# Kernel optimization log

Hardware: AMD Instinct MI355X
Metric: run time of the kernel (lower is better)

Reference implementation:

```python
import jax, jax.numpy as jnp
import numpy as np

N_HEAD = 16
D_MODEL = 1024
D_K = D_MODEL // N_HEAD  # 64
NEG = -1000000000.0


def setup_inputs() -> dict:
    key = jax.random.key(0)
    ks = jax.random.split(key, 7)
    B, L = 4, 2048
    q = jax.random.normal(ks[0], (B, L, D_MODEL), dtype=jnp.float32)
    k = jax.random.normal(ks[1], (B, L, D_MODEL), dtype=jnp.float32)
    v = jax.random.normal(ks[2], (B, L, D_MODEL), dtype=jnp.float32)
    mask = jnp.ones((B, L, L), dtype=jnp.int32)
    s = 1.0 / np.sqrt(D_MODEL)
    w_q = jax.random.normal(ks[3], (D_MODEL, D_MODEL), dtype=jnp.float32) * s
    w_k = jax.random.normal(ks[4], (D_MODEL, D_MODEL), dtype=jnp.float32) * s
    w_v = jax.random.normal(ks[5], (D_MODEL, D_MODEL), dtype=jnp.float32) * s
    w_o = jax.random.normal(ks[6], (D_MODEL, D_MODEL), dtype=jnp.float32) * s
    return {"q": q, "k": k, "v": v, "w_q": w_q, "w_k": w_k, "w_v": w_v, "w_o": w_o, "mask": mask}


def reference(q, k, v, w_q, w_k, w_v, w_o, mask):
    B, Lq, _ = q.shape
    temperature = jnp.asarray(D_K, q.dtype) ** 0.5
    # Projections (Linear, no bias): x @ W^T, then split heads -> [B, H, L, d_k]
    qh = (q @ w_q.T).reshape(B, Lq, N_HEAD, D_K).transpose(0, 2, 1, 3)
    kh = (k @ w_k.T).reshape(B, -1, N_HEAD, D_K).transpose(0, 2, 1, 3)
    vh = (v @ w_v.T).reshape(B, -1, N_HEAD, D_K).transpose(0, 2, 1, 3)
    # Scaled dot-product attention, full [B, H, Lq, Lk] scores materialized
    attn = jnp.einsum("bhqd,bhkd->bhqk", qh / temperature, kh)
    attn = jnp.where(mask[:, None, :, :] == 0, NEG, attn)
    attn = jax.nn.softmax(attn, axis=-1)  # dropout is identity in eval mode
    out = jnp.einsum("bhqk,bhkd->bhqd", attn, vh)
    out = out.transpose(0, 2, 1, 3).reshape(B, Lq, D_MODEL)
    return out @ w_o.T
```

## Files before the change

### kernel.cpp

```cpp
#include <hip/hip_runtime.h>
#include <stdint.h>

typedef float  f32x4  __attribute__((ext_vector_type(4)));
typedef __bf16 bf16x8 __attribute__((ext_vector_type(8)));
typedef __bf16 bf16x4 __attribute__((ext_vector_type(4)));
typedef short  s16x8  __attribute__((ext_vector_type(8)));
typedef short  s16x4  __attribute__((ext_vector_type(4)));
typedef unsigned int   u32;
typedef unsigned short u16;
typedef u32 u32x2 __attribute__((ext_vector_type(2)));

#define DM 1024
#define LQ 2048
#define NH 16

__device__ __forceinline__ u16 f2bf(float f) {
    unsigned int u = __builtin_bit_cast(unsigned int, f);
    u += 0x7FFFu + ((u >> 16) & 1u);
    return (u16)(u >> 16);
}

__device__ __forceinline__ float fexp2(float x) {
#if __has_builtin(__builtin_amdgcn_exp2f)
    return __builtin_amdgcn_exp2f(x);
#else
    return exp2f(x);
#endif
}

__device__ __forceinline__ u32 cvtpk(float lo, float hi) {
    u32 r;
    asm("v_cvt_pk_bf16_f32 %0, %1, %2" : "=v"(r) : "v"(lo), "v"(hi));
    return r;
}

__device__ __forceinline__ float max3f(float a, float b, float c) {
    float r;
    asm("v_max3_f32 %0, %1, %2, %3" : "=v"(r) : "v"(a), "v"(b), "v"(c));
    return r;
}

__device__ __forceinline__ f32x4 mfma32(s16x8 a, s16x8 b, f32x4 c) {
    return __builtin_amdgcn_mfma_f32_16x16x32_bf16(
        __builtin_bit_cast(bf16x8, a), __builtin_bit_cast(bf16x8, b), c, 0, 0, 0);
}

#if __has_builtin(__builtin_amdgcn_mfma_f32_16x16x16_bf16)
__device__ __forceinline__ f32x4 mfma16(s16x4 a, s16x4 b, f32x4 c) {
    return __builtin_amdgcn_mfma_f32_16x16x16_bf16(
        __builtin_bit_cast(bf16x4, a), __builtin_bit_cast(bf16x4, b), c, 0, 0, 0);
}
#else
__device__ __forceinline__ f32x4 mfma16(s16x4 a, s16x4 b, f32x4 c) {
    return __builtin_amdgcn_mfma_f32_16x16x16bf16_1k(a, b, c, 0, 0, 0);
}
#endif

#define GLD16(gp, lp) __builtin_amdgcn_global_load_lds( \
    (__attribute__((address_space(1))) void*)(gp),      \
    (__attribute__((address_space(3))) void*)(lp), 16, 0, 0)

__global__ void k_mask_check(const int4* __restrict__ m4, int n4, int* flag) {
    bool z = false;
    for (int i = blockIdx.x * blockDim.x + threadIdx.x; i < n4;
         i += gridDim.x * blockDim.x) {
        int4 v = m4[i];
        if (v.x == 0 || v.y == 0 || v.z == 0 || v.w == 0) z = true;
    }
    if (__ballot(z)) {
        if ((threadIdx.x & 63) == 0) atomicAnd(flag, 0);
    }
}

__global__ void k_cvt_all(const float4* __restrict__ q,  const float4* __restrict__ k,
                          const float4* __restrict__ v,  const float4* __restrict__ wq,
                          const float4* __restrict__ wk, const float4* __restrict__ wv,
                          const float4* __restrict__ wo,
                          uint64_t* xq, uint64_t* xk, uint64_t* xv,
                          uint64_t* bwq, uint64_t* bwk, uint64_t* bwv, uint64_t* bwo,
                          int* flag)
{
    if (blockIdx.x == 0 && threadIdx.x == 0) *flag = 1;
    const int NX = 2097152, NW = 262144;
    const int total = 3 * NX + 4 * NW;
    const int stride = gridDim.x * blockDim.x;
    for (int idx = blockIdx.x * blockDim.x + threadIdx.x; idx < total; idx += stride) {
        const float4* s; uint64_t* d; int off;
        if (idx < 3 * NX) {
            int ji = idx >> 21;
            off = idx & (NX - 1);
            s = ji == 0 ? q : ji == 1 ? k : v;
            d = ji == 0 ? xq : ji == 1 ? xk : xv;
        } else {
            int r = idx - 3 * NX;
            int ji = r >> 18;
            off = r & (NW - 1);
            s = ji == 0 ? wq : ji == 1 ? wk : ji == 2 ? wv : wo;
            d = ji == 0 ? bwq : ji == 1 ? bwk : ji == 2 ? bwv : bwo;
        }
        float4 f = s[off];
        union { u16 u[4]; uint64_t qq; } rr;
        rr.u[0] = f2bf(f.x); rr.u[1] = f2bf(f.y);
        rr.u[2] = f2bf(f.z); rr.u[3] = f2bf(f.w);
        d[off] = rr.qq;
    }
}

template <int MODE>
__global__ __launch_bounds__(256) void k_gemm(
    const u16* __restrict__ A, const u16* __restrict__ Bw,
    u16* __restrict__ Cb, float* __restrict__ Cf, float scale)
{
    constexpr int K = 1024;
    __shared__ char lA[128 * 32 * 2];
    __shared__ char lB[128 * 32 * 2];
    const int t = threadIdx.x, l = t & 63, w = t >> 6;
    const int q = l & 15, g = l >> 4;
    const int m0 = blockIdx.y * 128, n0 = blockIdx.x * 128;
    const int wr = (w >> 1) * 64, wc = (w & 1) * 64;

    f32x4 acc[4][4];
#pragma unroll
    for (int i = 0; i < 4; i++)
#pragma unroll
        for (int j = 0; j < 4; j++) acc[i][j] = (f32x4){0.f, 0.f, 0.f, 0.f};

    for (int k0 = 0; k0 < K; k0 += 32) {
#pragma unroll
        for (int c = 0; c < 2; c++) {
            int i = c * 256 + t;
            int row = i >> 2, sl = i & 3;
            int ss = sl ^ (row & 3);
            GLD16(A  + (size_t)(m0 + row) * K + k0 + ss * 8, lA + (i - l) * 16);
            GLD16(Bw + (size_t)(n0 + row) * K + k0 + ss * 8, lB + (i - l) * 16);
        }
        __syncthreads();
        s16x8 af[4], bfr[4];
#pragma unroll
        for (int mt = 0; mt < 4; mt++) {
            int r = wr + mt * 16 + q;
            af[mt] = *(const s16x8*)(lA + r * 64 + ((g ^ (r & 3)) * 16));
        }
#pragma unroll
        for (int nt = 0; nt < 4; nt++) {
            int r = wc + nt * 16 + q;
            bfr[nt] = *(const s16x8*)(lB + r * 64 + ((g ^ (r & 3)) * 16));
        }
#pragma unroll
        for (int mt = 0; mt < 4; mt++)
#pragma unroll
            for (int nt = 0; nt < 4; nt++)
                acc[mt][nt] = mfma32(bfr[nt], af[mt], acc[mt][nt]);
        __syncthreads();
    }

#pragma unroll
    for (int mt = 0; mt < 4; mt++) {
        int m = m0 + wr + mt * 16 + q;
#pragma unroll
        for (int nt = 0; nt < 4; nt++) {
            int n = n0 + wc + nt * 16 + g * 4;
            f32x4 a = acc[mt][nt];
            if (MODE == 0) {
                int bb = m >> 11, row = m & 2047;
                int h = n >> 6, d = n & 63;
                s16x4 pk;
#pragma unroll
                for (int j = 0; j < 4; j++) pk[j] = (short)f2bf(a[j] * scale);
                *(s16x4*)(Cb + (((size_t)(bb * NH + h) * LQ + row) << 6) + d) = pk;
            } else {
                f32x4 o;
#pragma unroll
                for (int j = 0; j < 4; j++) o[j] = a[j] * scale;
                *(f32x4*)(Cf + (size_t)m * DM + n) = o;
            }
        }
    }
}

__global__ __launch_bounds__(256, 2) void k_attn(
    const u16* __restrict__ Qh, const u16* __restrict__ Kh,
    const u16* __restrict__ Vh, u16* __restrict__ ctx,
    const int* __restrict__ mask, const int* __restrict__ flag)
{
    __shared__ char lds[32768];
    char* lK0 = lds;
    char* lV0 = lds + 16384;
    const int t = threadIdx.x, l = t & 63, w = t >> 6;
    const int g = l >> 4, q = l & 15;
    const int p = blockIdx.x;
    const int bh = (p & 7) * 8 + ((p >> 3) >> 3);
    const int qt = ((p >> 3) & 7) * 256;
    const int allones = *flag;
    const size_t base = (size_t)bh * LQ * 64;
    const int dg = t & 15, kg = t >> 4;

    s16x8 qf[4][2];
#pragma unroll
    for (int qh = 0; qh < 4; qh++)
#pragma unroll
        for (int kh = 0; kh < 2; kh++)
            qf[qh][kh] = *(const s16x8*)(
                Qh + base + (size_t)(qt + w * 64 + qh * 16 + q) * 64 + kh * 32 + g * 8);

    f32x4 oacc[4][4];
#pragma unroll
    for (int qh = 0; qh < 4; qh++)
#pragma unroll
        for (int dt = 0; dt < 4; dt++) oacc[qh][dt] = (f32x4){0.f, 0.f, 0.f, 0.f};
    float mrow[4] = {-1e30f, -1e30f, -1e30f, -1e30f};
    float lrow[4] = {0.f, 0.f, 0.f, 0.f};

    auto stageK = [&](int kt, int b) {
#pragma unroll
        for (int c = 0; c < 2; c++) {
            int i = c * 256 + t;
            int row = i >> 3, sl = i & 7;
            GLD16(Kh + base + (size_t)(kt + row) * 64 + ((sl ^ (row & 7)) * 8),
                  lK0 + b * 8192 + (i - l) * 16);
        }
    };
    auto loadV = [&](int kt, s16x4* vr) {
#pragma unroll
        for (int j = 0; j < 4; j++)
            vr[j] = *(const s16x4*)(Vh + base + (size_t)(kt + kg * 4 + j) * 64 + dg * 4);
    };
    auto writeV = [&](const s16x4* vr, int b) {
        u32x2 vv[4];
#pragma unroll
        for (int j = 0; j < 4; j++) vv[j] = __builtin_bit_cast(u32x2, vr[j]);
#pragma unroll
        for (int jj = 0; jj < 4; jj++) {
            int d = dg * 4 + jj;
            u32 a0 = vv[0][jj >> 1], a1 = vv[1][jj >> 1];
            u32 a2 = vv[2][jj >> 1], a3 = vv[3][jj >> 1];
            u32 w0, w1;
            if (jj & 1) { w0 = (a0 >> 16) | (a1 & 0xffff0000u);
                          w1 = (a2 >> 16) | (a3 & 0xffff0000u); }
            else        { w0 = (a0 & 0xffffu) | (a1 << 16);
                          w1 = (a2 & 0xffffu) | (a3 << 16); }
            u32x2 pw = {w0, w1};
            *(s16x4*)(lV0 + b * 8192 + d * 128 + ((kg ^ (d & 15)) * 8)) =
                __builtin_bit_cast(s16x4, pw);
        }
    };

    {
        s16x4 vr[4];
        stageK(0, 0);
        loadV(0, vr);
        writeV(vr, 0);
    }

    int cur = 0;
    for (int kt = 0; kt < LQ; kt += 64) {
        __syncthreads();
        const bool more = (kt + 64) < LQ;
        s16x4 vr[4];
        if (more) {
            stageK(kt + 64, cur ^ 1);
            loadV(kt + 64, vr);
        }

        f32x4 sc[4][4];
#pragma unroll
        for (int qh = 0; qh < 4; qh++)
#pragma unroll
            for (int ct = 0; ct < 4; ct++) sc[qh][ct] = (f32x4){0.f, 0.f, 0.f, 0.f};
        __builtin_amdgcn_s_setprio(1);
#pragma unroll
        for (int ct = 0; ct < 4; ct++) {
            int kc = ct * 16 + q;
#pragma unroll
            for (int kh = 0; kh < 2; kh++) {
                s16x8 kf = *(const s16x8*)(lK0 + cur * 8192 + kc * 128 +
                                           (((kh * 4 + g) ^ (kc & 7)) * 16));
#pragma unroll
                for (int qh = 0; qh < 4; qh++)
                    sc[qh][ct] = mfma32(kf, qf[qh][kh], sc[qh][ct]);
            }
        }
        __builtin_amdgcn_s_setprio(0);

        if (!allones) {
            int b = bh >> 4;
#pragma unroll
            for (int qh = 0; qh < 4; qh++)
#pragma unroll
                for (int ct = 0; ct < 4; ct++)
#pragma unroll
                    for (int r = 0; r < 4; r++) {
                        int qr = qt + w * 64 + qh * 16 + q;
                        int kc = kt + ct * 16 + g * 4 + r;
                        if (mask[(size_t)(b * LQ + qr) * LQ + kc] == 0)
                            sc[qh][ct][r] = -1e9f;
                    }
        }

        float pm[4];
#pragma unroll
        for (int qh = 0; qh < 4; qh++) {
            float m0 = max3f(sc[qh][0][0], sc[qh][0][1], sc[qh][0][2]);
            m0 = max3f(m0, sc[qh][0][3], sc[qh][1][0]);
            m0 = max3f(m0, sc[qh][1][1], sc[qh][1][2]);
            m0 = max3f(m0, sc[qh][1][3], sc[qh][2][0]);
            m0 = max3f(m0, sc[qh][2][1], sc[qh][2][2]);
            m0 = max3f(m0, sc[qh][2][3], sc[qh][3][0]);
            m0 = max3f(m0, sc[qh][3][1], sc[qh][3][2]);
            m0 = fmaxf(m0, sc[qh][3][3]);
            m0 = fmaxf(m0, __shfl_xor(m0, 16, 64));
            m0 = fmaxf(m0, __shfl_xor(m0, 32, 64));
            pm[qh] = m0;
        }
        bool ok = pm[0] <= mrow[0] + 8.f;
        ok = ok && (pm[1] <= mrow[1] + 8.f);
        ok = ok && (pm[2] <= mrow[2] + 8.f);
        ok = ok && (pm[3] <= mrow[3] + 8.f);
        if (!__all(ok)) {
#pragma unroll
            for (int qh = 0; qh < 4; qh++) {
                float nm = fmaxf(mrow[qh], pm[qh]);
                float corr = fexp2(mrow[qh] - nm);
                mrow[qh] = nm;
                lrow[qh] *= corr;
                float cv[4];
#pragma unroll
                for (int r = 0; r < 4; r++) cv[r] = __shfl(corr, g * 4 + r, 64);
#pragma unroll
                for (int dt = 0; dt < 4; dt++)
#pragma unroll
                    for (int r = 0; r < 4; r++) oacc[qh][dt][r] *= cv[r];
            }
        }
        s16x4 pa[4][4];
#pragma unroll
        for (int qh = 0; qh < 4; qh++) {
            float rs = 0.f;
#pragma unroll
            for (int ct = 0; ct < 4; ct++)
#pragma unroll
                for (int r = 0; r < 4; r++) {
                    float e = fexp2(sc[qh][ct][r] - mrow[qh]);
                    sc[qh][ct][r] = e;
                    rs += e;
                }
            rs += __shfl_xor(rs, 16, 64);
            rs += __shfl_xor(rs, 32, 64);
            lrow[qh] += rs;
#pragma unroll
            for (int s = 0; s < 4; s++) {
                u32x2 pw;
                pw.x = cvtpk(sc[qh][s][0], sc[qh][s][1]);
                pw.y = cvtpk(sc[qh][s][2], sc[qh][s][3]);
                pa[qh][s] = __builtin_bit_cast(s16x4, pw);
            }
        }

        __builtin_amdgcn_s_setprio(1);
#pragma unroll
        for (int dt = 0; dt < 4; dt++) {
#pragma unroll
            for (int s = 0; s < 4; s++) {
                s16x4 vf = *(const s16x4*)(lV0 + cur * 8192 + (dt * 16 + q) * 128 +
                                           (((s * 4 + g) ^ q) * 8));
#pragma unroll
                for (int qh = 0; qh < 4; qh++)
                    oacc[qh][dt] = mfma16(pa[qh][s], vf, oacc[qh][dt]);
            }
        }
        __builtin_amdgcn_s_setprio(0);

        if (more) writeV(vr, cur ^ 1);
        cur ^= 1;
    }

    __syncthreads();
    char* eb = lds + w * 8192;
#pragma unroll
    for (int qh = 0; qh < 4; qh++) {
        float lv[4];
#pragma unroll
        for (int r = 0; r < 4; r++) lv[r] = 1.f / __shfl(lrow[qh], g * 4 + r, 64);
#pragma unroll
        for (int dt = 0; dt < 4; dt++)
#pragma unroll
            for (int r = 0; r < 4; r++) {
                int row = qh * 16 + g * 4 + r;
                int cb = ((dt * 16 + q) * 2) ^ ((row & 7) << 4);
                *(u16*)(eb + row * 128 + cb) = f2bf(oacc[qh][dt][r] * lv[r]);
            }
    }
    __syncthreads();
    const int b = bh >> 4, h = bh & 15;
    const int token = qt + w * 64 + l;
    u16* gp = ctx + (size_t)(b * LQ + token) * DM + h * 64;
#pragma unroll
    for (int j = 0; j < 8; j++) {
        int cb = (j * 16) ^ ((l & 7) << 4);
        *(s16x8*)(gp + j * 8) = *(const s16x8*)(eb + l * 128 + cb);
    }
}

extern "C" void kernel_launch(void* const* d_in, const int* in_sizes, int n_in,
                              void* d_out, int out_size, void* d_ws, size_t ws_size,
                              hipStream_t stream)
{
    const float* q  = (const float*)d_in[0];
    const float* k  = (const float*)d_in[1];
    const float* v  = (const float*)d_in[2];
    const float* wq = (const float*)d_in[3];
    const float* wk = (const float*)d_in[4];
    const float* wv = (const float*)d_in[5];
    const float* wo = (const float*)d_in[6];
    const int* mask = (const int*)d_in[7];

    char* ws = (char*)d_ws;
    const size_t SX = (size_t)8192 * 1024 * 2;
    const size_t SW = (size_t)1024 * 1024 * 2;
    u16* xq  = (u16*)(ws);
    u16* xk  = (u16*)(ws + SX);
    u16* xv  = (u16*)(ws + 2 * SX);
    u16* bwq = (u16*)(ws + 3 * SX);
    u16* bwk = (u16*)(ws + 3 * SX + SW);
    u16* bwv = (u16*)(ws + 3 * SX + 2 * SW);
    u16* bwo = (u16*)(ws + 3 * SX + 3 * SW);
    u16* Qh  = (u16*)(ws + 3 * SX + 4 * SW);
    u16* Kh  = (u16*)(ws + 4 * SX + 4 * SW);
    u16* Vh  = (u16*)(ws + 5 * SX + 4 * SW);
    u16* ctx = (u16*)(ws + 6 * SX + 4 * SW);
    int* flag = (int*)(ws + 7 * SX + 4 * SW);

    k_cvt_all<<<2048, 256, 0, stream>>>(
        (const float4*)q, (const float4*)k, (const float4*)v,
        (const float4*)wq, (const float4*)wk, (const float4*)wv, (const float4*)wo,
        (uint64_t*)xq, (uint64_t*)xk, (uint64_t*)xv,
        (uint64_t*)bwq, (uint64_t*)bwk, (uint64_t*)bwv, (uint64_t*)bwo, flag);
    k_mask_check<<<2048, 256, 0, stream>>>((const int4*)mask,
                                           (4 * 2048 * 2048) / 4, flag);

    dim3 gg(8, 64);
    k_gemm<0><<<gg, 256, 0, stream>>>(xq, bwq, Qh, nullptr, 0.18033688011112042f);
    k_gemm<0><<<gg, 256, 0, stream>>>(xk, bwk, Kh, nullptr, 1.0f);
    k_gemm<0><<<gg, 256, 0, stream>>>(xv, bwv, Vh, nullptr, 1.0f);

    k_attn<<<512, 256, 0, stream>>>(Qh, Kh, Vh, ctx, mask, flag);

    k_gemm<1><<<gg, 256, 0, stream>>>(ctx, bwo, nullptr, (float*)d_out, 1.0f);
}
```

Measured before the change: 271.1 us.

## Batch QKV projections into one launch, swizzle tile order, use v_perm for V transpose

The three Q/K/V projection GEMMs become a single launch that uses blockIdx.z to pick the input, weight and output, relying on the contiguous workspace layout. The 2D grid is flattened and remapped so consecutive blocks share weight column tiles and nearby rows, which should improve L2 reuse. In the attention kernel's V staging, the shift/mask bf16 interleave becomes v_perm_b32 byte permutes. The intent is to cut launch overhead and tail effects and to trim ALU work, at the cost of depending on fixed buffer strides.

Result: faster. 250.2 us (-7.7%).

```diff
diff --git a/kernel.cpp b/kernel.cpp
--- a/kernel.cpp
+++ b/kernel.cpp
@@ -37,6 +37,12 @@
 __device__ __forceinline__ float max3f(float a, float b, float c) {
     float r;
     asm("v_max3_f32 %0, %1, %2, %3" : "=v"(r) : "v"(a), "v"(b), "v"(c));
+    return r;
+}
+
+__device__ __forceinline__ u32 permb(u32 b, u32 a, u32 sel) {
+    u32 r;
+    asm("v_perm_b32 %0, %1, %2, %3" : "=v"(r) : "v"(b), "v"(a), "s"(sel));
     return r;
 }
 
@@ -108,15 +114,23 @@
 
 template <int MODE>
 __global__ __launch_bounds__(256) void k_gemm(
-    const u16* __restrict__ A, const u16* __restrict__ Bw,
-    u16* __restrict__ Cb, float* __restrict__ Cf, float scale)
+    const u16* __restrict__ A0, const u16* __restrict__ Bw0,
+    u16* __restrict__ Cb0, float* __restrict__ Cf, float scale)
 {
     constexpr int K = 1024;
     __shared__ char lA[128 * 32 * 2];
     __shared__ char lB[128 * 32 * 2];
     const int t = threadIdx.x, l = t & 63, w = t >> 6;
     const int q = l & 15, g = l >> 4;
-    const int m0 = blockIdx.y * 128, n0 = blockIdx.x * 128;
+    const int z = (MODE == 0) ? blockIdx.z : 0;
+    const u16* A  = A0  + (size_t)z * 8388608;
+    const u16* Bw = Bw0 + (size_t)z * 1048576;
+    u16* Cb = (MODE == 0) ? Cb0 + (size_t)z * 8388608 : nullptr;
+    const float scl = (MODE == 0 && z != 0) ? 1.0f : scale;
+    const int lin = blockIdx.x;
+    const int ytile = ((lin & 7) << 3) | ((lin >> 3) & 7);
+    const int xtile = lin >> 6;
+    const int m0 = ytile * 128, n0 = xtile * 128;
     const int wr = (w >> 1) * 64, wc = (w & 1) * 64;
 
     f32x4 acc[4][4];
@@ -166,12 +180,12 @@
                 int h = n >> 6, d = n & 63;
                 s16x4 pk;
 #pragma unroll
-                for (int j = 0; j < 4; j++) pk[j] = (short)f2bf(a[j] * scale);
+                for (int j = 0; j < 4; j++) pk[j] = (short)f2bf(a[j] * scl);
                 *(s16x4*)(Cb + (((size_t)(bb * NH + h) * LQ + row) << 6) + d) = pk;
             } else {
                 f32x4 o;
 #pragma unroll
-                for (int j = 0; j < 4; j++) o[j] = a[j] * scale;
+                for (int j = 0; j < 4; j++) o[j] = a[j] * scl;
                 *(f32x4*)(Cf + (size_t)m * DM + n) = o;
             }
         }
@@ -226,6 +240,7 @@
             vr[j] = *(const s16x4*)(Vh + base + (size_t)(kt + kg * 4 + j) * 64 + dg * 4);
     };
     auto writeV = [&](const s16x4* vr, int b) {
+        const u32 selLO = 0x05040100u, selHI = 0x07060302u;
         u32x2 vv[4];
 #pragma unroll
         for (int j = 0; j < 4; j++) vv[j] = __builtin_bit_cast(u32x2, vr[j]);
@@ -234,12 +249,8 @@
             int d = dg * 4 + jj;
             u32 a0 = vv[0][jj >> 1], a1 = vv[1][jj >> 1];
             u32 a2 = vv[2][jj >> 1], a3 = vv[3][jj >> 1];
-            u32 w0, w1;
-            if (jj & 1) { w0 = (a0 >> 16) | (a1 & 0xffff0000u);
-                          w1 = (a2 >> 16) | (a3 & 0xffff0000u); }
-            else        { w0 = (a0 & 0xffffu) | (a1 << 16);
-                          w1 = (a2 & 0xffffu) | (a3 << 16); }
-            u32x2 pw = {w0, w1};
+            u32 sel = (jj & 1) ? selHI : selLO;
+            u32x2 pw = {permb(a1, a0, sel), permb(a3, a2, sel)};
             *(s16x4*)(lV0 + b * 8192 + d * 128 + ((kg ^ (d & 15)) * 8)) =
                 __builtin_bit_cast(s16x4, pw);
         }
@@ -438,12 +449,10 @@
     k_mask_check<<<2048, 256, 0, stream>>>((const int4*)mask,
                                            (4 * 2048 * 2048) / 4, flag);
 
-    dim3 gg(8, 64);
-    k_gemm<0><<<gg, 256, 0, stream>>>(xq, bwq, Qh, nullptr, 0.18033688011112042f);
-    k_gemm<0><<<gg, 256, 0, stream>>>(xk, bwk, Kh, nullptr, 1.0f);
-    k_gemm<0><<<gg, 256, 0, stream>>>(xv, bwv, Vh, nullptr, 1.0f);
+    k_gemm<0><<<dim3(512, 1, 3), 256, 0, stream>>>(xq, bwq, Qh, nullptr,
+                                                   0.18033688011112042f);
 
     k_attn<<<512, 256, 0, stream>>>(Qh, Kh, Vh, ctx, mask, flag);
 
-    k_gemm<1><<<gg, 256, 0, stream>>>(ctx, bwo, nullptr, (float*)d_out, 1.0f);
-}
+    k_gemm<1><<<dim3(512), 256, 0, stream>>>(ctx, bwo, nullptr, (float*)d_out, 1.0f);
+}
```
